# Optimization experiments

Measured on AMD Instinct MI355X. Metric: run time of the kernel, lower is better.

The kernel has to match this reference:

```python
import jax, jax.numpy as jnp
import numpy as np

N_EXPERTS = 8
FDIM1 = 1024
FDIM2 = 512
NUM_CLASSES = 64
BATCH = 16384


def setup_inputs() -> dict:
    key = jax.random.key(0)
    k1, k2, k3, k4, k5, k6 = jax.random.split(key, 6)
    s1 = 1.0 / np.sqrt(FDIM1)
    s2 = 1.0 / np.sqrt(FDIM2)
    return {
        "domain": jax.random.randint(k1, (BATCH,), 0, N_EXPERTS, dtype=jnp.int64 if jax.config.jax_enable_x64 else jnp.int32),
        "x": jax.random.normal(k2, (BATCH, FDIM1), dtype=jnp.float32),
        "W1": jax.random.uniform(k3, (N_EXPERTS, FDIM1, FDIM2), jnp.float32, -s1, s1),
        "b1": jax.random.uniform(k4, (N_EXPERTS, FDIM2), jnp.float32, -s1, s1),
        "W2": jax.random.uniform(k5, (N_EXPERTS, FDIM2, NUM_CLASSES), jnp.float32, -s2, s2),
        "b2": jax.random.uniform(k6, (N_EXPERTS, NUM_CLASSES), jnp.float32, -s2, s2),
    }


def reference(domain, x, W1, b1, W2, b2):
    # All-expert 2-layer MLP (matches torch loop-over-experts + stack):
    # h: [B, E, fdim2]
    h = jax.nn.relu(jnp.einsum("bf,efh->beh", x, W1) + b1[None, :, :])
    # logits: [B, E, C]
    logits = jnp.einsum("beh,ehc->bec", h, W2) + b2[None, :, :]
    # Gather the expert selected by each sample's domain, then softmax.
    sel = jnp.take_along_axis(logits, domain[:, None, None].astype(jnp.int32), axis=1)[:, 0, :]
    return jax.nn.softmax(sel, axis=-1)
```

## Files before the change

### kernel.cpp

```cpp
#include <hip/hip_runtime.h>
#include <hip/hip_bf16.h>

#define BATCH 16384
#define F1    1024
#define F2    512
#define NCLS  64
#define NEXP  8
#define BPAD  (BATCH + NEXP*128)
#define NBM   136
#define NBG1  544
#define NBG2  272

typedef __attribute__((ext_vector_type(8))) short short8;
typedef __attribute__((ext_vector_type(4))) float float4v;

#define O_META   0
#define O_BEXP   4096
#define O_ORDER  8192
#define O_XPH    131072
#define O_XPL    (O_XPH + 35651584)
#define O_W1H    (O_XPL + 35651584)
#define O_W1L    (O_W1H + 8388608)
#define O_W2H    (O_W1L + 8388608)
#define O_W2L    (O_W2H + 524288)
#define O_HH     (O_W2L + 524288)
#define O_HL     (O_HH + 17825792)

__device__ inline short bf16_rn(float f) {
    unsigned u = __builtin_bit_cast(unsigned, f);
    u = (u + 0x7fffu + ((u >> 16) & 1u)) >> 16;
    return (short)u;
}
__device__ inline float bf16_up(short h) {
    return __builtin_bit_cast(float, ((unsigned)(unsigned short)h) << 16);
}
__device__ inline void split2(float v, short& hi, short& lo) {
    hi = bf16_rn(v);
    lo = bf16_rn(v - bf16_up(hi));
}
__device__ inline float4v mfma16(short8 a, short8 b, float4v c) {
    return __builtin_amdgcn_mfma_f32_16x16x32_bf16(a, b, c, 0, 0, 0);
}
__device__ inline void glds16(const void* g, void* l) {
    __builtin_amdgcn_global_load_lds((const __attribute__((address_space(1))) void*)g,
                                     (__attribute__((address_space(3))) void*)l,
                                     16, 0, 0);
}

__global__ void dael_init(const int* __restrict__ domain, int* meta, int* order) {
    __shared__ int hc[NEXP];
    const int b = blockIdx.x, t = threadIdx.x;
    const int i = b * 256 + t;
    if (i < BPAD) order[i] = -1;
    if (b < 64) {
        if (t < NEXP) hc[t] = 0;
        __syncthreads();
        atomicAdd(&hc[domain[i]], 1);
        __syncthreads();
        if (t < NEXP) meta[64 + b * NEXP + t] = hc[t];
    }
}

__global__ void dael_plan(int* meta, int* bexp) {
    __shared__ int cnt[NEXP], soff[NEXP + 1];
    const int t = threadIdx.x;
    if (t < NEXP) {
        int s = 0;
        for (int b = 0; b < 64; ++b) s += meta[64 + b * NEXP + t];
        cnt[t] = s;
    }
    __syncthreads();
    if (t == 0) {
        int acc = 0;
        for (int e = 0; e < NEXP; ++e) {
            soff[e] = acc;
            meta[16 + e] = acc * 128;
            meta[8 + e] = 0;
            acc += (cnt[e] + 127) >> 7;
        }
        soff[NEXP] = acc;
    }
    __syncthreads();
    for (int i = t; i < NBM; i += 256) {
        int ee = -1;
        #pragma unroll
        for (int e = 0; e < NEXP; ++e)
            if (i >= soff[e] && i < soff[e + 1]) ee = e;
        bexp[i] = ee;
    }
}

__global__ void dael_scatter(const int* __restrict__ domain, int* meta, int* order) {
    __shared__ int lc[NEXP], lb[NEXP];
    const int t = threadIdx.x;
    const int i = blockIdx.x * 256 + t;
    if (t < NEXP) lc[t] = 0;
    __syncthreads();
    const int d = domain[i];
    const int r = atomicAdd(&lc[d], 1);
    __syncthreads();
    if (t < NEXP && lc[t] > 0) lb[t] = atomicAdd(&meta[8 + t], lc[t]);
    __syncthreads();
    order[meta[16 + d] + lb[d] + r] = i;
}

#define NPX 1088
#define NPW1 1024
#define NPW2 64
__global__ __launch_bounds__(256)
void dael_pack(const int* __restrict__ order,
               const float* __restrict__ x, short* xph, short* xpl,
               const float* __restrict__ W1, short* w1h, short* w1l,
               const float* __restrict__ W2, short* w2h, short* w2l) {
    const int b = blockIdx.x, t = threadIdx.x;
    if (b < NPX) {
        const int mb = b >> 3, kg = b & 7;
        const int r = t & 127;
        const int samp = order[mb * 128 + r];
        #pragma unroll
        for (int kl = 0; kl < 4; ++kl) {
            const int ks = kg * 4 + kl;
            const size_t tb = (size_t)(mb * 32 + ks) * 4096;
            #pragma unroll
            for (int sl = 0; sl < 2; ++sl) {
                const int s = t + sl * 256;
                const int q = s >> 7;
                short8 vh = {}, vl = {};
                if (samp >= 0) {
                    const float* src = x + (size_t)samp * F1 + ks * 32 + q * 8;
                    float4 f0 = *(const float4*)src;
                    float4 f1 = *(const float4*)(src + 4);
                    float va[8] = {f0.x, f0.y, f0.z, f0.w, f1.x, f1.y, f1.z, f1.w};
                    #pragma unroll
                    for (int i = 0; i < 8; ++i) { short h, l; split2(va[i], h, l); vh[i] = h; vl[i] = l; }
                }
                *(short8*)(xph + tb + s * 8) = vh;
                *(short8*)(xpl + tb + s * 8) = vl;
            }
        }
    } else if (b < NPX + NPW1) {
        const int b2 = b - NPX;
        const int e = b2 >> 7, strip = (b2 >> 5) & 3, ks = b2 & 31;
        const size_t tb = (size_t)((e * 4 + strip) * 32 + ks) * 4096;
        #pragma unroll
        for (int sl = 0; sl < 2; ++sl) {
            const int s = t + sl * 256;
            const int q = s >> 7, r = s & 127;
            const int n = strip * 128 + r;
            short8 vh, vl;
            #pragma unroll
            for (int jj = 0; jj < 8; ++jj) {
                const int k = ks * 32 + q * 8 + jj;
                float v = W1[((size_t)(e * F1 + k)) * F2 + n];
                short h, l; split2(v, h, l); vh[jj] = h; vl[jj] = l;
            }
            *(short8*)(w1h + tb + s * 8) = vh;
            *(short8*)(w1l + tb + s * 8) = vl;
        }
    } else {
        const int b3 = b - NPX - NPW1;
        const int e = b3 >> 3, ks = b3 & 7;
        const size_t tb = (size_t)(e * 8 + ks) * 4096;
        #pragma unroll
        for (int sl = 0; sl < 2; ++sl) {
            const int s = t + sl * 256;
            const int q = s >> 6, c = s & 63;
            short8 vh, vl;
            #pragma unroll
            for (int jj = 0; jj < 8; ++jj) {
                const int k = ks * 64 + q * 8 + jj;
                float v = W2[((size_t)(e * F2 + k)) * NCLS + c];
                short h, l; split2(v, h, l); vh[jj] = h; vl[jj] = l;
            }
            *(short8*)(w2h + tb + s * 8) = vh;
            *(short8*)(w2l + tb + s * 8) = vl;
        }
    }
}

__global__ __launch_bounds__(256)
void dael_gemm1(const int* __restrict__ bexp,
                const short* __restrict__ xph, const short* __restrict__ xpl,
                const short* __restrict__ w1h, const short* __restrict__ w1l,
                const float* __restrict__ b1,
                short* __restrict__ hh, short* __restrict__ hl) {
    const int L = blockIdx.x;
    const int xcd = L & 7, j = L >> 3;
    const int mb = xcd * 17 + (j % 17);
    const int strip = j / 17;
    const int e = bexp[mb];
    if (e < 0) return;
    const int tid = threadIdx.x;
    const int lane = tid & 63, wv = tid >> 6;
    const int quad = lane >> 4, lrow = lane & 15;
    const int r0w = (wv & 1) * 64, c0w = (wv >> 1) * 64;

    __shared__ __align__(16) char SMc[65536];

    const short* Ah = xph + (size_t)(mb * 32) * 4096 + tid * 8;
    const short* Al = xpl + (size_t)(mb * 32) * 4096 + tid * 8;
    const short* Bh = w1h + (size_t)((e * 4 + strip) * 32) * 4096 + tid * 8;
    const short* Bl = w1l + (size_t)((e * 4 + strip) * 32) * 4096 + tid * 8;
    const int d0 = tid * 16;

    float4v acc[4][4] = {};
    int offa[4], offb[4];
    #pragma unroll
    for (int i = 0; i < 4; ++i) offa[i] = quad * 2048 + (r0w + i * 16 + lrow) * 16;
    #pragma unroll
    for (int jj = 0; jj < 4; ++jj) offb[jj] = 16384 + quad * 2048 + (c0w + jj * 16 + lrow) * 16;

    {
        glds16(Ah,        SMc + d0);
        glds16(Ah + 2048, SMc + 4096 + d0);
        glds16(Al,        SMc + 8192 + d0);
        glds16(Al + 2048, SMc + 12288 + d0);
        glds16(Bh,        SMc + 16384 + d0);
        glds16(Bh + 2048, SMc + 20480 + d0);
        glds16(Bl,        SMc + 24576 + d0);
        glds16(Bl + 2048, SMc + 28672 + d0);
    }

    for (int ks = 0; ks < 32; ++ks) {
        __syncthreads();
        if (ks + 1 < 32) {
            const int so = (ks + 1) * 4096;
            const int db = ((ks + 1) & 1) * 32768;
            glds16(Ah + so,        SMc + db + d0);
            glds16(Ah + so + 2048, SMc + db + 4096 + d0);
            glds16(Al + so,        SMc + db + 8192 + d0);
            glds16(Al + so + 2048, SMc + db + 12288 + d0);
            glds16(Bh + so,        SMc + db + 16384 + d0);
            glds16(Bh + so + 2048, SMc + db + 20480 + d0);
            glds16(Bl + so,        SMc + db + 24576 + d0);
            glds16(Bl + so + 2048, SMc + db + 28672 + d0);
        }
        const int db = (ks & 1) * 32768;
        short8 ah[4], al[4];
        #pragma unroll
        for (int i = 0; i < 4; ++i) {
            ah[i] = *(const short8*)(SMc + db + offa[i]);
            al[i] = *(const short8*)(SMc + db + 8192 + offa[i]);
        }
        #pragma unroll
        for (int jj = 0; jj < 4; ++jj) {
            short8 bh = *(const short8*)(SMc + db + offb[jj]);
            short8 bl = *(const short8*)(SMc + db + 8192 + offb[jj]);
            #pragma unroll
            for (int i = 0; i < 4; ++i) {
                acc[i][jj] = mfma16(ah[i], bh, acc[i][jj]);
                acc[i][jj] = mfma16(ah[i], bl, acc[i][jj]);
                acc[i][jj] = mfma16(al[i], bh, acc[i][jj]);
            }
        }
    }

    float bv[4];
    #pragma unroll
    for (int jj = 0; jj < 4; ++jj)
        bv[jj] = b1[e * F2 + strip * 128 + c0w + jj * 16 + lrow];
    short* T = (short*)SMc;
    #pragma unroll
    for (int plane = 0; plane < 2; ++plane) {
        __syncthreads();
        #pragma unroll
        for (int i = 0; i < 4; ++i)
            #pragma unroll
            for (int jj = 0; jj < 4; ++jj)
                #pragma unroll
                for (int r = 0; r < 4; ++r) {
                    const int m = r0w + i * 16 + quad * 4 + r;
                    const int n = c0w + jj * 16 + lrow;
                    float hv = fmaxf(acc[i][jj][r] + bv[jj], 0.f);
                    short hi = bf16_rn(hv);
                    T[m * 136 + n] = plane ? bf16_rn(hv - bf16_up(hi)) : hi;
                }
        __syncthreads();
        short* dst = plane ? hl : hh;
        #pragma unroll
        for (int u = 0; u < 8; ++u) {
            const int sidx = tid + 256 * u;
            const int g = sidx >> 6, m64 = sidx & 63;
            const int mloc = g >> 4, ksl = (g >> 3) & 1, q = g & 7;
            const int m = mloc * 64 + m64;
            const int n = ksl * 64 + q * 8;
            const size_t off = ((size_t)((mb * 2 + mloc) * 8 + strip * 2 + ksl)) * 4096
                               + q * 512 + m64 * 8;
            *(short8*)(dst + off) = *(const short8*)&T[m * 136 + n];
        }
    }
}

__global__ __launch_bounds__(256)
void dael_gemm2(const int* __restrict__ order, const int* __restrict__ bexp,
                const short* __restrict__ hh, const short* __restrict__ hl,
                const short* __restrict__ w2h, const short* __restrict__ w2l,
                const float* __restrict__ b2, float* __restrict__ out) {
    const int b = blockIdx.x;
    const int e = bexp[b >> 1];
    if (e < 0) return;
    const int p0 = b * 64;
    const int tid = threadIdx.x;
    const int lane = tid & 63, wv = tid >> 6;
    const int quad = lane >> 4, lrow = lane & 15;

    __shared__ __align__(16) char SM2[65536];
    __shared__ float inv[64];

    const short* Ah = hh + (size_t)(b * 8) * 4096 + tid * 8;
    const short* Al = hl + (size_t)(b * 8) * 4096 + tid * 8;
    const short* Bh = w2h + (size_t)(e * 8) * 4096 + tid * 8;
    const short* Bl = w2l + (size_t)(e * 8) * 4096 + tid * 8;
    const int d0 = tid * 16;

    float4v acc[4] = {};

    {
        glds16(Ah,        SM2 + d0);
        glds16(Ah + 2048, SM2 + 4096 + d0);
        glds16(Al,        SM2 + 8192 + d0);
        glds16(Al + 2048, SM2 + 12288 + d0);
        glds16(Bh,        SM2 + 16384 + d0);
        glds16(Bh + 2048, SM2 + 20480 + d0);
        glds16(Bl,        SM2 + 24576 + d0);
        glds16(Bl + 2048, SM2 + 28672 + d0);
    }

    for (int ks = 0; ks < 8; ++ks) {
        __syncthreads();
        if (ks + 1 < 8) {
            const int so = (ks + 1) * 4096;
            const int db = ((ks + 1) & 1) * 32768;
            glds16(Ah + so,        SM2 + db + d0);
            glds16(Ah + so + 2048, SM2 + db + 4096 + d0);
            glds16(Al + so,        SM2 + db + 8192 + d0);
            glds16(Al + so + 2048, SM2 + db + 12288 + d0);
            glds16(Bh + so,        SM2 + db + 16384 + d0);
            glds16(Bh + so + 2048, SM2 + db + 20480 + d0);
            glds16(Bl + so,        SM2 + db + 24576 + d0);
            glds16(Bl + so + 2048, SM2 + db + 28672 + d0);
        }
        const int db = (ks & 1) * 32768;
        #pragma unroll
        for (int ksub = 0; ksub < 2; ++ksub) {
            const int qa = (ksub * 4 + quad) * 1024;
            const int ao = db + qa + (wv * 16 + lrow) * 16;
            short8 ahf = *(const short8*)(SM2 + ao);
            short8 alf = *(const short8*)(SM2 + 8192 + ao);
            #pragma unroll
            for (int jj = 0; jj < 4; ++jj) {
                const int bo = db + 16384 + qa + (jj * 16 + lrow) * 16;
                short8 bh = *(const short8*)(SM2 + bo);
                short8 bl = *(const short8*)(SM2 + 8192 + bo);
                acc[jj] = mfma16(ahf, bh, acc[jj]);
                acc[jj] = mfma16(ahf, bl, acc[jj]);
                acc[jj] = mfma16(alf, bh, acc[jj]);
            }
        }
    }

    __syncthreads();
    float* Lx = (float*)SM2;
    #pragma unroll
    for (int jj = 0; jj < 4; ++jj) {
        const int n = jj * 16 + lrow;
        const float bb = b2[e * NCLS + n];
        #pragma unroll
        for (int r = 0; r < 4; ++r)
            Lx[(wv * 16 + quad * 4 + r) * 68 + n] = acc[jj][r] + bb;
    }
    __syncthreads();
    if (tid < 64) {
        float mx = -3.402823466e38f;
        #pragma unroll 8
        for (int c = 0; c < NCLS; ++c) mx = fmaxf(mx, Lx[tid * 68 + c]);
        float s = 0.f;
        #pragma unroll 8
        for (int c = 0; c < NCLS; ++c) {
            float ev = __expf(Lx[tid * 68 + c] - mx);
            Lx[tid * 68 + c] = ev; s += ev;
        }
        inv[tid] = 1.f / s;
    }
    __syncthreads();
    const int r = tid >> 2, cs = (tid & 3) * 16;
    const int samp = order[p0 + r];
    if (samp >= 0) {
        const float sc = inv[r];
        #pragma unroll
        for (int q = 0; q < 4; ++q) {
            float4 v = *(const float4*)&Lx[r * 68 + cs + q * 4];
            v.x *= sc; v.y *= sc; v.z *= sc; v.w *= sc;
            *(float4*)(out + (size_t)samp * NCLS + cs + q * 4) = v;
        }
    }
}

extern "C" void kernel_launch(void* const* d_in, const int* in_sizes, int n_in,
                              void* d_out, int out_size, void* d_ws, size_t ws_size,
                              hipStream_t stream) {
    const int*   domain = (const int*)d_in[0];
    const float* x      = (const float*)d_in[1];
    const float* W1     = (const float*)d_in[2];
    const float* b1     = (const float*)d_in[3];
    const float* W2     = (const float*)d_in[4];
    const float* b2     = (const float*)d_in[5];
    float* out = (float*)d_out;

    char* ws = (char*)d_ws;
    int*   meta  = (int*)(ws + O_META);
    int*   bexp  = (int*)(ws + O_BEXP);
    int*   order = (int*)(ws + O_ORDER);
    short* xph   = (short*)(ws + O_XPH);
    short* xpl   = (short*)(ws + O_XPL);
    short* w1h   = (short*)(ws + O_W1H);
    short* w1l   = (short*)(ws + O_W1L);
    short* w2h   = (short*)(ws + O_W2H);
    short* w2l   = (short*)(ws + O_W2L);
    short* hh    = (short*)(ws + O_HH);
    short* hl    = (short*)(ws + O_HL);

    dael_init<<<68, 256, 0, stream>>>(domain, meta, order);
    dael_plan<<<1, 256, 0, stream>>>(meta, bexp);
    dael_scatter<<<64, 256, 0, stream>>>(domain, meta, order);
    dael_pack<<<NPX + NPW1 + NPW2, 256, 0, stream>>>(order, x, xph, xpl,
                                                     W1, w1h, w1l, W2, w2h, w2l);
    dael_gemm1<<<NBG1, 256, 0, stream>>>(bexp, xph, xpl, w1h, w1l, b1, hh, hl);
    dael_gemm2<<<NBG2, 256, 0, stream>>>(order, bexp, hh, hl, w2h, w2l, b2, out);
}
```

Before: 234.0 us.

## Split-phase LDS pipeline with fine-grained vmcnt waits and MFMA priority

New measurement: 231.7 us. No clear change (-1.0%).

```diff
diff --git a/kernel.cpp b/kernel.cpp
--- a/kernel.cpp
+++ b/kernel.cpp
@@ -219,31 +219,63 @@
         glds16(Bh + 2048, SMc + 20480 + d0);
         glds16(Bl,        SMc + 24576 + d0);
         glds16(Bl + 2048, SMc + 28672 + d0);
+        glds16(Ah + 4096,        SMc + 32768 + d0);
+        glds16(Ah + 4096 + 2048, SMc + 32768 + 4096 + d0);
+        glds16(Al + 4096,        SMc + 32768 + 8192 + d0);
+        glds16(Al + 4096 + 2048, SMc + 32768 + 12288 + d0);
     }
 
     for (int ks = 0; ks < 32; ++ks) {
-        __syncthreads();
+        const int db = (ks & 1) * 32768;
+        const int dn = db ^ 32768;
+
+        if (ks < 31) {
+            asm volatile("s_waitcnt vmcnt(4)" ::: "memory");
+        } else {
+            asm volatile("s_waitcnt vmcnt(0)" ::: "memory");
+        }
+        __builtin_amdgcn_s_barrier();
+        asm volatile("" ::: "memory");
         if (ks + 1 < 32) {
             const int so = (ks + 1) * 4096;
-            const int db = ((ks + 1) & 1) * 32768;
+            glds16(Bh + so,        SMc + dn + 16384 + d0);
+            glds16(Bh + so + 2048, SMc + dn + 20480 + d0);
+            glds16(Bl + so,        SMc + dn + 24576 + d0);
+            glds16(Bl + so + 2048, SMc + dn + 28672 + d0);
+        }
+        short8 ah[4], al[4];
+        #pragma unroll
+        for (int i = 0; i < 4; ++i) {
+            ah[i] = *(const short8*)(SMc + db + offa[i]);
+            al[i] = *(const short8*)(SMc + db + 8192 + offa[i]);
+        }
+        __builtin_amdgcn_s_setprio(1);
+        #pragma unroll
+        for (int jj = 0; jj < 2; ++jj) {
+            short8 bh = *(const short8*)(SMc + db + offb[jj]);
+            short8 bl = *(const short8*)(SMc + db + 8192 + offb[jj]);
+            #pragma unroll
+            for (int i = 0; i < 4; ++i) {
+                acc[i][jj] = mfma16(ah[i], bh, acc[i][jj]);
+                acc[i][jj] = mfma16(ah[i], bl, acc[i][jj]);
+                acc[i][jj] = mfma16(al[i], bh, acc[i][jj]);
+            }
+        }
+        __builtin_amdgcn_s_setprio(0);
+
+        asm volatile("" ::: "memory");
+        __builtin_amdgcn_s_barrier();
+        asm volatile("" ::: "memory");
+        if (ks + 2 < 32) {
+            const int so = (ks + 2) * 4096;
             glds16(Ah + so,        SMc + db + d0);
             glds16(Ah + so + 2048, SMc + db + 4096 + d0);
             glds16(Al + so,        SMc + db + 8192 + d0);
             glds16(Al + so + 2048, SMc + db + 12288 + d0);
-            glds16(Bh + so,        SMc + db + 16384 + d0);
-            glds16(Bh + so + 2048, SMc + db + 20480 + d0);
-            glds16(Bl + so,        SMc + db + 24576 + d0);
-            glds16(Bl + so + 2048, SMc + db + 28672 + d0);
-        }
-        const int db = (ks & 1) * 32768;
-        short8 ah[4], al[4];
-        #pragma unroll
-        for (int i = 0; i < 4; ++i) {
-            ah[i] = *(const short8*)(SMc + db + offa[i]);
-            al[i] = *(const short8*)(SMc + db + 8192 + offa[i]);
-        }
-        #pragma unroll
-        for (int jj = 0; jj < 4; ++jj) {
+        }
+        __builtin_amdgcn_s_setprio(1);
+        #pragma unroll
+        for (int jj = 2; jj < 4; ++jj) {
             short8 bh = *(const short8*)(SMc + db + offb[jj]);
             short8 bl = *(const short8*)(SMc + db + 8192 + offb[jj]);
             #pragma unroll
@@ -253,6 +285,7 @@
                 acc[i][jj] = mfma16(al[i], bh, acc[i][jj]);
             }
         }
+        __builtin_amdgcn_s_setprio(0);
     }
 
     float bv[4];
```

## Load GEMM1 A operand directly from global into registers, shrink LDS

Applied to the files above, without the earlier changes.

Result: no change. 236.3 us (+1.0%).

```diff
diff --git a/kernel.cpp b/kernel.cpp
--- a/kernel.cpp
+++ b/kernel.cpp
@@ -178,7 +178,7 @@
     }
 }
 
-__global__ __launch_bounds__(256)
+__global__ __launch_bounds__(256, 4)
 void dael_gemm1(const int* __restrict__ bexp,
                 const short* __restrict__ xph, const short* __restrict__ xpl,
                 const short* __restrict__ w1h, const short* __restrict__ w1l,
@@ -195,53 +195,48 @@
     const int quad = lane >> 4, lrow = lane & 15;
     const int r0w = (wv & 1) * 64, c0w = (wv >> 1) * 64;
 
-    __shared__ __align__(16) char SMc[65536];
-
-    const short* Ah = xph + (size_t)(mb * 32) * 4096 + tid * 8;
-    const short* Al = xpl + (size_t)(mb * 32) * 4096 + tid * 8;
+    __shared__ __align__(16) char SMc[36864];
+
+    const size_t abase = (size_t)(mb * 32) * 4096 + (size_t)(quad * 128 + r0w + lrow) * 8;
+    const short* AH = xph + abase;
+    const short* AL = xpl + abase;
     const short* Bh = w1h + (size_t)((e * 4 + strip) * 32) * 4096 + tid * 8;
     const short* Bl = w1l + (size_t)((e * 4 + strip) * 32) * 4096 + tid * 8;
     const int d0 = tid * 16;
 
     float4v acc[4][4] = {};
-    int offa[4], offb[4];
+    int offb[4];
     #pragma unroll
-    for (int i = 0; i < 4; ++i) offa[i] = quad * 2048 + (r0w + i * 16 + lrow) * 16;
-    #pragma unroll
-    for (int jj = 0; jj < 4; ++jj) offb[jj] = 16384 + quad * 2048 + (c0w + jj * 16 + lrow) * 16;
+    for (int jj = 0; jj < 4; ++jj) offb[jj] = quad * 2048 + (c0w + jj * 16 + lrow) * 16;
 
     {
-        glds16(Ah,        SMc + d0);
-        glds16(Ah + 2048, SMc + 4096 + d0);
-        glds16(Al,        SMc + 8192 + d0);
-        glds16(Al + 2048, SMc + 12288 + d0);
-        glds16(Bh,        SMc + 16384 + d0);
-        glds16(Bh + 2048, SMc + 20480 + d0);
-        glds16(Bl,        SMc + 24576 + d0);
-        glds16(Bl + 2048, SMc + 28672 + d0);
+        glds16(Bh,        SMc + d0);
+        glds16(Bh + 2048, SMc + 4096 + d0);
+        glds16(Bl,        SMc + 8192 + d0);
+        glds16(Bl + 2048, SMc + 12288 + d0);
     }
 
     for (int ks = 0; ks < 32; ++ks) {
+        short8 ah[4], al[4];
+        {
+            const int sa = ks * 4096;
+            #pragma unroll
+            for (int i = 0; i < 4; ++i) {
+                ah[i] = *(const short8*)(AH + sa + i * 128);
+                al[i] = *(const short8*)(AL + sa + i * 128);
+            }
+        }
         __syncthreads();
         if (ks + 1 < 32) {
             const int so = (ks + 1) * 4096;
-            const int db = ((ks + 1) & 1) * 32768;
-            glds16(Ah + so,        SMc + db + d0);
-            glds16(Ah + so + 2048, SMc + db + 4096 + d0);
-            glds16(Al + so,        SMc + db + 8192 + d0);
-            glds16(Al + so + 2048, SMc + db + 12288 + d0);
-            glds16(Bh + so,        SMc + db + 16384 + d0);
-            glds16(Bh + so + 2048, SMc + db + 20480 + d0);
-            glds16(Bl + so,        SMc + db + 24576 + d0);
-            glds16(Bl + so + 2048, SMc + db + 28672 + d0);
-        }
-        const int db = (ks & 1) * 32768;
-        short8 ah[4], al[4];
-        #pragma unroll
-        for (int i = 0; i < 4; ++i) {
-            ah[i] = *(const short8*)(SMc + db + offa[i]);
-            al[i] = *(const short8*)(SMc + db + 8192 + offa[i]);
-        }
+            const int dn = ((ks + 1) & 1) * 16384;
+            glds16(Bh + so,        SMc + dn + d0);
+            glds16(Bh + so + 2048, SMc + dn + 4096 + d0);
+            glds16(Bl + so,        SMc + dn + 8192 + d0);
+            glds16(Bl + so + 2048, SMc + dn + 12288 + d0);
+        }
+        const int db = (ks & 1) * 16384;
+        __builtin_amdgcn_s_setprio(1);
         #pragma unroll
         for (int jj = 0; jj < 4; ++jj) {
             short8 bh = *(const short8*)(SMc + db + offb[jj]);
@@ -253,6 +248,7 @@
                 acc[i][jj] = mfma16(al[i], bh, acc[i][jj]);
             }
         }
+        __builtin_amdgcn_s_setprio(0);
     }
 
     float bv[4];
```
